# Kernel tuning notes

Measured on AMD Instinct MI355X. Metric: run time of the kernel, lower is better.

The kernel has to match this reference:

```python
import jax, jax.numpy as jnp
import numpy as np

HIDDEN = 768
HEADS = 12
HEAD_DIM = 64
SEQ = 512
DS_K = 64  # downsampling_k
EPS = 1e-6


def setup_inputs() -> dict:
    key = jax.random.key(0)
    ks = jax.random.split(key, 16)
    B = 32
    sd = 1.0 / DS_K
    glorot = jax.nn.initializers.lecun_normal()  # flax default_kernel_init
    inp = {
        "query": jax.random.normal(ks[0], (B, SEQ, HIDDEN), jnp.float32),
        "key": jax.random.normal(ks[1], (B, SEQ, HIDDEN), jnp.float32),
        "value": jax.random.normal(ks[2], (B, SEQ, HIDDEN), jnp.float32),
        "step": 0,
        # learned Linformer-style downsampling projections [k, s]
        "W_kds": sd * jax.random.normal(ks[3], (DS_K, SEQ), jnp.float32),
        "W_vds": sd * jax.random.normal(ks[4], (DS_K, SEQ), jnp.float32),
        # DenseGeneral qkv kernels [d, n, h] and biases [n, h]
        "Wq": glorot(ks[5], (HIDDEN, HEADS, HEAD_DIM), jnp.float32),
        "bq": jnp.zeros((HEADS, HEAD_DIM), jnp.float32),
        "Wk": glorot(ks[6], (HIDDEN, HEADS, HEAD_DIM), jnp.float32),
        "bk": jnp.zeros((HEADS, HEAD_DIM), jnp.float32),
        "Wv": glorot(ks[7], (HIDDEN, HEADS, HEAD_DIM), jnp.float32),
        "bv": jnp.zeros((HEADS, HEAD_DIM), jnp.float32),
        # out projection contracts (n, h) -> hidden
        "Wout": glorot(ks[8], (HEADS * HEAD_DIM, HIDDEN), jnp.float32).reshape(HEADS, HEAD_DIM, HIDDEN),
        "bout": jnp.zeros((HIDDEN,), jnp.float32),
    }
    return inp


def reference(query, key, value, step, W_kds, W_vds, Wq, bq, Wk, bk, Wv, bv, Wout, bout):
    # Linformer-style downsample of keys/values along sequence: [b,s,d] -> [b,k,d]
    key_ds = jnp.einsum("ks,bsd->bkd", W_kds, key)
    val_ds = jnp.einsum("ks,bsd->bkd", W_vds, value)

    # per-head projections
    queries = jnp.einsum("bqd,dnh->bqnh", query, Wq) + bq    # [b,q,n,h]
    keys = jnp.einsum("bkd,dnh->bknh", key_ds, Wk) + bk      # [b,k,n,h]
    values = jnp.einsum("bkd,dnh->bknh", val_ds, Wv) + bv    # [b,k,n,h]

    # kernelized linear attention with elu feature map (mask=False path)
    phi_q = jax.nn.elu(queries) + 1.0
    phi_k = jax.nn.elu(keys) + 1.0
    s = jnp.einsum("bknd,bknh->bndh", phi_k, values)          # [b,n,h,h] KV state
    z = jnp.sum(phi_k, axis=1)                                 # [b,n,h]
    qs = jnp.einsum("bqnd,bndh->bqnh", phi_q, s)
    qz = jnp.einsum("bqnd,bnd->bqn", phi_q, z) + EPS
    a_v = qs / qz[..., None]                                   # [b,q,n,h]

    out = jnp.einsum("bqnh,nhD->bqD", a_v, Wout) + bout        # [b,q,hidden]
    return out
```

## Files before the change

kernel.cpp:

```cpp
#include <hip/hip_runtime.h>

typedef unsigned short u16;
typedef u16 u16x8 __attribute__((ext_vector_type(8)));
typedef __bf16 bf16;
typedef bf16 bf16x8 __attribute__((ext_vector_type(8)));
typedef float f32x4 __attribute__((ext_vector_type(4)));

__device__ __forceinline__ float bf2f(u16 v) {
  union { unsigned u; float f; } x; x.u = ((unsigned)v) << 16; return x.f;
}
__device__ __forceinline__ u16 f2bf(float f) {
  union { float f; unsigned u; } x; x.f = f;
  unsigned u = x.u;
  u += 0x7fffu + ((u >> 16) & 1u);
  return (u16)(u >> 16);
}

#define GLDS16(g, l) __builtin_amdgcn_global_load_lds( \
    (const __attribute__((address_space(1))) unsigned int*)(const void*)(g), \
    (__attribute__((address_space(3))) unsigned int*)(void*)(l), 16, 0, 0)

__global__ __launch_bounds__(256, 4) void prepds_k(
    const float* __restrict__ Wq, const float* __restrict__ Wk,
    const float* __restrict__ Wv, const float* __restrict__ Wout,
    const float* __restrict__ query,
    const float* __restrict__ W_kds, const float* __restrict__ W_vds,
    const float* __restrict__ b0, const float* __restrict__ b1,
    const float* __restrict__ b2, const float* __restrict__ b3,
    const float* __restrict__ key, const float* __restrict__ value,
    u16* __restrict__ WT, u16* __restrict__ q_bf,
    u16* __restrict__ dstB, u16* __restrict__ key_ds)
{
  __shared__ u16 S[64 * 256];
  const int blk = blockIdx.x;
  const int t = threadIdx.x;

  if (blk < 768) {
    const int nt = (blk % 12) * 64;
    const int yb = blk / 12;
    const int pair = yb >> 5, b = yb & 31;
    const float* src = (pair ? value : key) + (size_t)b * 512 * 768;
    const float* W32 = pair ? W_vds : W_kds;
    u16* dst = key_ds + (size_t)pair * 1572864 + (size_t)b * 49152;
    const int wave = t >> 6, lane = t & 63;
    const int bn = lane;
    const int kl = wave * 64;
    const int sw = (bn & 7) << 3;
    const float* bcol = src + nt + bn;
    const int wm = (wave >> 1) * 32, wn = (wave & 1) * 32;
    const int lrow = lane & 15, quad = lane >> 4;
    f32x4 acc[2][2] = {};

    auto st16 = [&](const float* buf, int off) {
      #pragma unroll
      for (int g = 0; g < 2; ++g) {
        u16x8 wv;
        #pragma unroll
        for (int i = 0; i < 8; ++i) wv[i] = f2bf(buf[g * 8 + i]);
        *(u16x8*)&S[bn * 256 + ((kl + off + g * 8) ^ sw)] = wv;
      }
    };

    #pragma unroll
    for (int ph = 0; ph < 2; ++ph) {
      const int kb = ph * 256;
      if (ph) __syncthreads();
      float ba[16], bb[16];
      #pragma unroll
      for (int i = 0; i < 16; ++i) ba[i] = bcol[(size_t)(kb + kl + i) * 768];
      #pragma unroll
      for (int i = 0; i < 16; ++i) bb[i] = bcol[(size_t)(kb + kl + 16 + i) * 768];
      st16(ba, 0);
      #pragma unroll
      for (int i = 0; i < 16; ++i) ba[i] = bcol[(size_t)(kb + kl + 32 + i) * 768];
      st16(bb, 16);
      #pragma unroll
      for (int i = 0; i < 16; ++i) bb[i] = bcol[(size_t)(kb + kl + 48 + i) * 768];
      st16(ba, 32);
      st16(bb, 48);
      __syncthreads();
      #pragma unroll
      for (int step = 0; step < 8; ++step) {
        bf16x8 av2[2], bv[2];
        #pragma unroll
        for (int i = 0; i < 2; ++i) {
          const float* wr = &W32[(size_t)(wm + i * 16 + lrow) * 512 + kb + step * 32 + quad * 8];
          f32x4 w0 = *(const f32x4*)wr;
          f32x4 w1 = *(const f32x4*)(wr + 4);
          u16x8 aw;
          #pragma unroll
          for (int jj = 0; jj < 4; ++jj) { aw[jj] = f2bf(w0[jj]); aw[4 + jj] = f2bf(w1[jj]); }
          av2[i] = *(bf16x8*)&aw;
        }
        #pragma unroll
        for (int j = 0; j < 2; ++j) {
          const int n = wn + j * 16 + lrow;
          bv[j] = *(const bf16x8*)&S[n * 256 + ((step * 32 + quad * 8) ^ ((n & 7) << 3))];
        }
        #pragma unroll
        for (int i = 0; i < 2; ++i)
          #pragma unroll
          for (int j = 0; j < 2; ++j)
            acc[i][j] = __builtin_amdgcn_mfma_f32_16x16x32_bf16(av2[i], bv[j], acc[i][j], 0, 0, 0);
      }
    }
    #pragma unroll
    for (int i = 0; i < 2; ++i)
      #pragma unroll
      for (int j = 0; j < 2; ++j) {
        const int col = nt + wn + j * 16 + lrow;
        #pragma unroll
        for (int r = 0; r < 4; ++r) {
          const int row = wm + i * 16 + quad * 4 + r;
          dst[(size_t)row * 768 + col] = f2bf(acc[i][j][r]);
        }
      }
  } else if (blk < 1344) {
    u16 (*T)[72] = (u16(*)[72])S;
    const int tb = blk - 768;
    const int bz = tb / 144, rr = tb % 144;
    const int r0 = (rr / 12) * 64, c0 = (rr % 12) * 64;
    const float* W = (bz == 0) ? Wq : (bz == 1) ? Wk : (bz == 2) ? Wv : Wout;
    u16* O = WT + (size_t)bz * 768 * 768;
    #pragma unroll
    for (int p = 0; p < 2; ++p) {
      int v = t + p * 256;
      int r = v / 8, c = (v % 8) * 8;
      f32x4 x0 = *(const f32x4*)&W[(size_t)(r0 + r) * 768 + c0 + c];
      f32x4 x1 = *(const f32x4*)&W[(size_t)(r0 + r) * 768 + c0 + c + 4];
      #pragma unroll
      for (int i = 0; i < 4; ++i) { T[r][c + i] = f2bf(x0[i]); T[r][c + 4 + i] = f2bf(x1[i]); }
    }
    __syncthreads();
    #pragma unroll
    for (int p = 0; p < 2; ++p) {
      int v = t + p * 256;
      int r = v / 8, c = (v % 8) * 8;
      u16x8 tv;
      #pragma unroll
      for (int i = 0; i < 8; ++i) tv[i] = T[c + i][r];
      *(u16x8*)&O[(size_t)(c0 + r) * 768 + r0 + c] = tv;
    }
  } else if (blk < 7488) {
    const size_t i = (size_t)(blk - 1344) * 256 + t;
    f32x4 a = *(const f32x4*)&query[i * 8];
    f32x4 b = *(const f32x4*)&query[i * 8 + 4];
    u16x8 w;
    #pragma unroll
    for (int j = 0; j < 4; ++j) { w[j] = f2bf(a[j]); w[4 + j] = f2bf(b[j]); }
    *(u16x8*)&q_bf[i * 8] = w;
  } else {
    const int i = (blk - 7488) * 256 + t;
    if (i < 3072) {
      int s = i / 768, si = i % 768;
      const float* src = (s == 0) ? b0 : (s == 1) ? b1 : (s == 2) ? b2 : b3;
      dstB[i] = f2bf(src[si]);
    }
  }
}

template<int ACT, bool OF32>
__global__ __launch_bounds__(256) void gemm97_k(
    const u16* __restrict__ A, int lda,
    const u16* __restrict__ Bt, int ldb,
    void* __restrict__ Craw, int ldc,
    const u16* __restrict__ bias, int K)
{
  __shared__ u16 As[128 * 32];
  __shared__ u16 Bs[128 * 32];
  const int mt = blockIdx.x * 128, nt = blockIdx.y * 128;
  const int t = threadIdx.x, wave = t >> 6, lane = t & 63;
  const int wm = (wave >> 1) * 64, wn = (wave & 1) * 64;
  const int lrow = lane & 15, quad = lane >> 4;
  f32x4 acc[4][4] = {};

  for (int k0 = 0; k0 < K; k0 += 32) {
    __syncthreads();
    #pragma unroll
    for (int p = 0; p < 2; ++p) {
      const int s = wave * 128 + p * 64 + lane;
      const int r = s >> 2, c = (s & 3) * 8;
      const int lb = (wave * 128 + p * 64) * 8;
      GLDS16(&A[(size_t)(mt + r) * lda + k0 + c], &As[lb]);
      GLDS16(&Bt[(size_t)(nt + r) * ldb + k0 + c], &Bs[lb]);
    }
    __syncthreads();

    bf16x8 av[4], bv[4];
    #pragma unroll
    for (int i = 0; i < 4; ++i) av[i] = *(const bf16x8*)&As[(wm + i * 16 + lrow) * 32 + quad * 8];
    #pragma unroll
    for (int j = 0; j < 4; ++j) bv[j] = *(const bf16x8*)&Bs[(wn + j * 16 + lrow) * 32 + quad * 8];
    #pragma unroll
    for (int i = 0; i < 4; ++i)
      #pragma unroll
      for (int j = 0; j < 4; ++j)
        acc[i][j] = __builtin_amdgcn_mfma_f32_16x16x32_bf16(av[i], bv[j], acc[i][j], 0, 0, 0);
  }

  #pragma unroll
  for (int i = 0; i < 4; ++i) {
    #pragma unroll
    for (int j = 0; j < 4; ++j) {
      const int col = nt + wn + j * 16 + lrow;
      const float badd = bias ? bf2f(bias[col]) : 0.0f;
      #pragma unroll
      for (int r = 0; r < 4; ++r) {
        const int row = mt + wm + i * 16 + quad * 4 + r;
        float v = acc[i][j][r] + badd;
        if constexpr (ACT == 1) v = v > 0.0f ? v + 1.0f : __expf(v);
        if constexpr (OF32) ((float*)Craw)[(size_t)row * ldc + col] = v;
        else                ((u16*)Craw)[(size_t)row * ldc + col] = f2bf(v);
      }
    }
  }
}

template<int BM, int BN, int BK, int WM, int WN>
__global__ __launch_bounds__(256) void gemmkv_k(
    const u16* __restrict__ A, int lda,
    const u16* __restrict__ B, int ldb,
    u16* __restrict__ C, int ldc,
    const u16* __restrict__ bias,
    int K,
    long long offA_b, long long offB_b, long long offC_b, long long offBias_b)
{
  constexpr int LDSK = BK + 8;
  __shared__ u16 As[BM][LDSK];
  __shared__ u16 Bs[BN][LDSK];
  const int bb = blockIdx.z;
  A += bb * offA_b; B += bb * offB_b; C += bb * offC_b; bias += bb * offBias_b;
  const int mt = blockIdx.x * BM;
  const int nt = blockIdx.y * BN;
  const int t = threadIdx.x;
  const int wave = t >> 6, lane = t & 63;
  constexpr int WAVES_N = BN / WN;
  const int wm = (wave / WAVES_N) * WM;
  const int wn = (wave % WAVES_N) * WN;
  constexpr int FM = WM / 16, FN = WN / 16;
  const int lrow = lane & 15, quad = lane >> 4;
  f32x4 acc[FM][FN] = {};

  for (int k0 = 0; k0 < K; k0 += BK) {
    __syncthreads();
    #pragma unroll
    for (int p = 0; p < (BM * BK / 8) / 256; ++p) {
      int v = t + p * 256;
      int r = v / (BK / 8), c = (v % (BK / 8)) * 8;
      *(u16x8*)&As[r][c] = *(const u16x8*)&A[(size_t)(mt + r) * lda + k0 + c];
    }
    #pragma unroll
    for (int p = 0; p < (BN * BK / 8) / 256; ++p) {
      int v = t + p * 256;
      int r = v / (BK / 8), c = (v % (BK / 8)) * 8;
      *(u16x8*)&Bs[r][c] = *(const u16x8*)&B[(size_t)(nt + r) * ldb + k0 + c];
    }
    __syncthreads();
    bf16x8 av[FM], bv[FN];
    #pragma unroll
    for (int i = 0; i < FM; ++i) av[i] = *(const bf16x8*)&As[wm + i * 16 + lrow][quad * 8];
    #pragma unroll
    for (int j = 0; j < FN; ++j) bv[j] = *(const bf16x8*)&Bs[wn + j * 16 + lrow][quad * 8];
    #pragma unroll
    for (int i = 0; i < FM; ++i)
      #pragma unroll
      for (int j = 0; j < FN; ++j)
        acc[i][j] = __builtin_amdgcn_mfma_f32_16x16x32_bf16(av[i], bv[j], acc[i][j], 0, 0, 0);
  }
  #pragma unroll
  for (int i = 0; i < FM; ++i)
    #pragma unroll
    for (int j = 0; j < FN; ++j) {
      const int col = nt + wn + j * 16 + lrow;
      const float badd = bf2f(bias[col]);
      #pragma unroll
      for (int r = 0; r < 4; ++r) {
        const int row = mt + wm + i * 16 + quad * 4 + r;
        float v = acc[i][j][r] + badd;
        if (bb == 0) v = v > 0.0f ? v + 1.0f : __expf(v);
        C[(size_t)row * ldc + col] = f2bf(v);
      }
    }
}

__global__ __launch_bounds__(256) void kv_state_k(
    const u16* __restrict__ phi_k, const u16* __restrict__ vals,
    u16* __restrict__ sT, float* __restrict__ z)
{
  __shared__ float pk[64][65];
  __shared__ float vv[64][65];
  const int x = blockIdx.x;
  const int b = x / 12, n = x % 12;
  const int t = threadIdx.x;
  const u16* pkg = phi_k + (size_t)b * 64 * 768 + n * 64;
  const u16* vvg = vals  + (size_t)b * 64 * 768 + n * 64;
  #pragma unroll
  for (int p = 0; p < 2; ++p) {
    int v = t + p * 256;
    int r = v / 8, c = (v % 8) * 8;
    u16x8 a  = *(const u16x8*)&pkg[(size_t)r * 768 + c];
    u16x8 bq = *(const u16x8*)&vvg[(size_t)r * 768 + c];
    #pragma unroll
    for (int i = 0; i < 8; ++i) { pk[r][c + i] = bf2f(a[i]); vv[r][c + i] = bf2f(bq[i]); }
  }
  __syncthreads();
  const int d0 = (t >> 4) * 4, h0 = (t & 15) * 4;
  float s4[4][4] = {};
  for (int k = 0; k < 64; ++k) {
    float pv[4], vb[4];
    #pragma unroll
    for (int i = 0; i < 4; ++i) { pv[i] = pk[k][d0 + i]; vb[i] = vv[k][h0 + i]; }
    #pragma unroll
    for (int i = 0; i < 4; ++i)
      #pragma unroll
      for (int j = 0; j < 4; ++j) s4[i][j] += pv[i] * vb[j];
  }
  const size_t base = (size_t)x * 4096;
  #pragma unroll
  for (int i = 0; i < 4; ++i)
    #pragma unroll
    for (int j = 0; j < 4; ++j)
      sT[base + (size_t)(h0 + j) * 64 + d0 + i] = f2bf(s4[i][j]);
  if (t < 64) {
    float zz = 0.f;
    for (int k = 0; k < 64; ++k) zz += pk[k][t];
    z[(size_t)x * 64 + t] = zz;
  }
}

__global__ __launch_bounds__(256) void attn_av_k(
    u16* __restrict__ phi_q, const u16* __restrict__ sT, const float* __restrict__ zbuf)
{
  __shared__ u16 As[64 * 72];
  __shared__ u16 Bs[64 * 72];
  __shared__ float zv[64];
  __shared__ float zpart[4][64];
  __shared__ float zq[64];
  const int x = blockIdx.x, y = blockIdx.y;
  const int b = y / 12, n = y % 12;
  const int t = threadIdx.x;
  u16* Abase = phi_q + (size_t)b * 512 * 768 + (size_t)x * 64 * 768 + n * 64;
  const u16* Bbase = sT + (size_t)y * 4096;
  if (t < 64) zv[t] = zbuf[(size_t)y * 64 + t];
  #pragma unroll
  for (int p = 0; p < 2; ++p) {
    int v = t + p * 256;
    int r = v >> 3, c = (v & 7) * 8;
    *(u16x8*)&As[r * 72 + c] = *(const u16x8*)&Abase[(size_t)r * 768 + c];
    *(u16x8*)&Bs[r * 72 + c] = *(const u16x8*)&Bbase[r * 64 + c];
  }
  __syncthreads();
  {
    int r = t & 63, seg = t >> 6;
    float s = 0.f;
    #pragma unroll
    for (int j = 0; j < 16; ++j) s += bf2f(As[r * 72 + seg * 16 + j]) * zv[seg * 16 + j];
    zpart[seg][r] = s;
  }
  __syncthreads();
  if (t < 64) {
    float s = zpart[0][t] + zpart[1][t] + zpart[2][t] + zpart[3][t];
    zq[t] = 1.0f / (s + 1e-6f);
  }
  const int wave = t >> 6, lane = t & 63;
  const int wm = (wave >> 1) * 32, wn = (wave & 1) * 32;
  const int lrow = lane & 15, quad = lane >> 4;
  f32x4 acc[2][2] = {};
  #pragma unroll
  for (int c = 0; c < 2; ++c) {
    bf16x8 av[2], bv[2];
    #pragma unroll
    for (int i = 0; i < 2; ++i) av[i] = *(const bf16x8*)&As[(wm + i * 16 + lrow) * 72 + c * 32 + quad * 8];
    #pragma unroll
    for (int j = 0; j < 2; ++j) bv[j] = *(const bf16x8*)&Bs[(wn + j * 16 + lrow) * 72 + c * 32 + quad * 8];
    #pragma unroll
    for (int i = 0; i < 2; ++i)
      #pragma unroll
      for (int j = 0; j < 2; ++j)
        acc[i][j] = __builtin_amdgcn_mfma_f32_16x16x32_bf16(av[i], bv[j], acc[i][j], 0, 0, 0);
  }
  __syncthreads();
  #pragma unroll
  for (int i = 0; i < 2; ++i)
    #pragma unroll
    for (int j = 0; j < 2; ++j) {
      const int col = wn + j * 16 + lrow;
      #pragma unroll
      for (int r = 0; r < 4; ++r) {
        const int row = wm + i * 16 + quad * 4 + r;
        Abase[(size_t)row * 768 + col] = f2bf(acc[i][j][r] * zq[row]);
      }
    }
}

__global__ void tagfill_k(float* out, float val, int n) {
  int i = blockIdx.x * 256 + threadIdx.x;
  if (i < n) out[i] = val;
}

extern "C" void kernel_launch(void* const* d_in, const int* in_sizes, int n_in,
                              void* d_out, int out_size, void* d_ws, size_t ws_size,
                              hipStream_t stream) {
  (void)out_size;
  float* out = (float*)d_out;

  int o;
  if (n_in >= 14 && in_sizes[3] == 1) o = 4;
  else if (n_in == 13) o = 3;
  else { tagfill_k<<<4, 256, 0, stream>>>(out, 77.0f, 1024); return; }
  if (in_sizes[0] != 12582912 || in_sizes[o + 0] != 32768 || in_sizes[o + 2] != 589824) {
    tagfill_k<<<4, 256, 0, stream>>>(out, 88.0f, 1024); return;
  }

  const float* query = (const float*)d_in[0];
  const float* key   = (const float*)d_in[1];
  const float* value = (const float*)d_in[2];
  const float* W_kds = (const float*)d_in[o + 0];
  const float* W_vds = (const float*)d_in[o + 1];
  const float* Wq   = (const float*)d_in[o + 2];
  const float* bq   = (const float*)d_in[o + 3];
  const float* Wk   = (const float*)d_in[o + 4];
  const float* bk   = (const float*)d_in[o + 5];
  const float* Wv   = (const float*)d_in[o + 6];
  const float* bv   = (const float*)d_in[o + 7];
  const float* Wout = (const float*)d_in[o + 8];
  const float* bout = (const float*)d_in[o + 9];

  const size_t NEED = 61478912;
  if (ws_size < NEED) { tagfill_k<<<4, 256, 0, stream>>>(out, 123.0f, 1024); return; }

  char* base = (char*)d_ws;
  u16*   WT     = (u16*)base;
  char*  Breg   = base + 4718592;
  u16*   q_bf   = (u16*)Breg;
  u16*   sT     = (u16*)Breg;
  float* zbuf   = (float*)(Breg + 3145728);
  u16*   phi_k  = (u16*)(Breg + 6291456);
  u16*   vals   = (u16*)(Breg + 9437184);
  u16*   phi_q  = (u16*)(base + 29884416);
  u16*   bias_c = (u16*)(base + 55181312);
  u16*   key_ds = (u16*)(base + 55187456);
  u16* a_v = phi_q;
  u16* WqT   = WT;
  u16* WkT   = WT + 768 * 768;
  u16* WoutT = WT + 3 * 768 * 768;
  u16* bq_c = bias_c, *bk_c = bias_c + 768, *bout_c = bias_c + 2304;

  prepds_k<<<7500, 256, 0, stream>>>(Wq, Wk, Wv, Wout, query, W_kds, W_vds,
                                     bq, bk, bv, bout, key, value,
                                     WT, q_bf, bias_c, key_ds);

  gemm97_k<1, false><<<dim3(128, 6), 256, 0, stream>>>(
      q_bf, 768, WqT, 768, phi_q, 768, bq_c, 768);

  gemmkv_k<64, 64, 32, 32, 32><<<dim3(32, 12, 2), 256, 0, stream>>>(
      key_ds, 768, WkT, 768, phi_k, 768, bk_c, 768,
      1572864, 589824, 1572864, 768);

  kv_state_k<<<dim3(384), 256, 0, stream>>>(phi_k, vals, sT, zbuf);

  attn_av_k<<<dim3(8, 384), 256, 0, stream>>>(phi_q, sT, zbuf);

  gemm97_k<0, true><<<dim3(128, 6), 256, 0, stream>>>(
      a_v, 768, WoutT, 768, out, 768, bout_c, 768);
}
```

Measured before the change: 316.9 us.

## Fuse K/V projection with KV-state kernel and rework downsample staging

Merges the per-head K/V projection GEMM and the KV-state/z reduction into one kernel per (batch, head), so phi_k and values stay in LDS and never round-trip through global memory. This also drops one launch and uses MFMA for the state outer product. The downsample path in the prep kernel now stages fp32 key/value tiles with async global-to-LDS loads and pre-converts the W_ds rows to bf16 in LDS. Downsample blocks are interleaved with the conversion blocks (every tenth block) to spread the heavy work across the grid. In exchange, the fused kernel runs only 384 blocks, and bf16 conversion now happens per LDS read during the MFMA loop.

```diff
diff --git a/kernel.cpp b/kernel.cpp
--- a/kernel.cpp
+++ b/kernel.cpp
@@ -1,6 +1,7 @@
 #include <hip/hip_runtime.h>
 
 typedef unsigned short u16;
+typedef u16 u16x4 __attribute__((ext_vector_type(4)));
 typedef u16 u16x8 __attribute__((ext_vector_type(8)));
 typedef __bf16 bf16;
 typedef bf16 bf16x8 __attribute__((ext_vector_type(8)));
@@ -20,7 +21,7 @@
     (const __attribute__((address_space(1))) unsigned int*)(const void*)(g), \
     (__attribute__((address_space(3))) unsigned int*)(void*)(l), 16, 0, 0)
 
-__global__ __launch_bounds__(256, 4) void prepds_k(
+__global__ __launch_bounds__(256) void prepds_k(
     const float* __restrict__ Wq, const float* __restrict__ Wk,
     const float* __restrict__ Wv, const float* __restrict__ Wout,
     const float* __restrict__ query,
@@ -31,78 +32,70 @@
     u16* __restrict__ WT, u16* __restrict__ q_bf,
     u16* __restrict__ dstB, u16* __restrict__ key_ds)
 {
-  __shared__ u16 S[64 * 256];
+  __shared__ char sm[50176];
   const int blk = blockIdx.x;
   const int t = threadIdx.x;
 
-  if (blk < 768) {
-    const int nt = (blk % 12) * 64;
-    const int yb = blk / 12;
+  if (blk % 10 == 0) {
+    const int id = blk / 10;
+    float* Sg = (float*)sm;
+    u16* Wbf = (u16*)(sm + 32768);
+    const int nt = (id % 12) * 64;
+    const int yb = id / 12;
     const int pair = yb >> 5, b = yb & 31;
     const float* src = (pair ? value : key) + (size_t)b * 512 * 768;
     const float* W32 = pair ? W_vds : W_kds;
     u16* dst = key_ds + (size_t)pair * 1572864 + (size_t)b * 49152;
     const int wave = t >> 6, lane = t & 63;
-    const int bn = lane;
-    const int kl = wave * 64;
-    const int sw = (bn & 7) << 3;
-    const float* bcol = src + nt + bn;
     const int wm = (wave >> 1) * 32, wn = (wave & 1) * 32;
     const int lrow = lane & 15, quad = lane >> 4;
+    const int gr = lane >> 4;
+    const int gc = (lane & 15) * 16;
+    const int wrow = t >> 5;
+    const int wcol = (t & 31) * 4;
     f32x4 acc[2][2] = {};
 
-    auto st16 = [&](const float* buf, int off) {
-      #pragma unroll
-      for (int g = 0; g < 2; ++g) {
-        u16x8 wv;
-        #pragma unroll
-        for (int i = 0; i < 8; ++i) wv[i] = f2bf(buf[g * 8 + i]);
-        *(u16x8*)&S[bn * 256 + ((kl + off + g * 8) ^ sw)] = wv;
-      }
-    };
-
-    #pragma unroll
-    for (int ph = 0; ph < 2; ++ph) {
-      const int kb = ph * 256;
-      if (ph) __syncthreads();
-      float ba[16], bb[16];
-      #pragma unroll
-      for (int i = 0; i < 16; ++i) ba[i] = bcol[(size_t)(kb + kl + i) * 768];
-      #pragma unroll
-      for (int i = 0; i < 16; ++i) bb[i] = bcol[(size_t)(kb + kl + 16 + i) * 768];
-      st16(ba, 0);
-      #pragma unroll
-      for (int i = 0; i < 16; ++i) ba[i] = bcol[(size_t)(kb + kl + 32 + i) * 768];
-      st16(bb, 16);
-      #pragma unroll
-      for (int i = 0; i < 16; ++i) bb[i] = bcol[(size_t)(kb + kl + 48 + i) * 768];
-      st16(ba, 32);
-      st16(bb, 48);
+    for (int ph = 0; ph < 4; ++ph) {
+      const int kb = ph * 128;
+      #pragma unroll
+      for (int j = 0; j < 8; ++j) {
+        const int idx = wave * 8 + j;
+        const float* gsrc = src + (size_t)(kb + idx * 4 + gr) * 768 + nt;
+        GLDS16((const char*)gsrc + gc, (char*)Sg + idx * 1024);
+      }
+      f32x4 wr[8];
+      #pragma unroll
+      for (int i = 0; i < 8; ++i)
+        wr[i] = *(const f32x4*)&W32[(size_t)(i * 8 + wrow) * 512 + kb + wcol];
+      #pragma unroll
+      for (int i = 0; i < 8; ++i) {
+        u16x4 wv4;
+        #pragma unroll
+        for (int q2 = 0; q2 < 4; ++q2) wv4[q2] = f2bf(wr[i][q2]);
+        *(u16x4*)&Wbf[(i * 8 + wrow) * 136 + wcol] = wv4;
+      }
       __syncthreads();
       #pragma unroll
-      for (int step = 0; step < 8; ++step) {
-        bf16x8 av2[2], bv[2];
-        #pragma unroll
-        for (int i = 0; i < 2; ++i) {
-          const float* wr = &W32[(size_t)(wm + i * 16 + lrow) * 512 + kb + step * 32 + quad * 8];
-          f32x4 w0 = *(const f32x4*)wr;
-          f32x4 w1 = *(const f32x4*)(wr + 4);
-          u16x8 aw;
+      for (int s = 0; s < 4; ++s) {
+        bf16x8 av[2], bv[2];
+        #pragma unroll
+        for (int i = 0; i < 2; ++i)
+          av[i] = *(const bf16x8*)&Wbf[(wm + i * 16 + lrow) * 136 + s * 32 + quad * 8];
+        #pragma unroll
+        for (int j = 0; j < 2; ++j) {
+          const int n2 = wn + j * 16 + lrow;
+          u16x8 bb;
           #pragma unroll
-          for (int jj = 0; jj < 4; ++jj) { aw[jj] = f2bf(w0[jj]); aw[4 + jj] = f2bf(w1[jj]); }
-          av2[i] = *(bf16x8*)&aw;
-        }
-        #pragma unroll
-        for (int j = 0; j < 2; ++j) {
-          const int n = wn + j * 16 + lrow;
-          bv[j] = *(const bf16x8*)&S[n * 256 + ((step * 32 + quad * 8) ^ ((n & 7) << 3))];
+          for (int e = 0; e < 8; ++e) bb[e] = f2bf(Sg[(s * 32 + quad * 8 + e) * 64 + n2]);
+          bv[j] = *(bf16x8*)&bb;
         }
         #pragma unroll
         for (int i = 0; i < 2; ++i)
           #pragma unroll
           for (int j = 0; j < 2; ++j)
-            acc[i][j] = __builtin_amdgcn_mfma_f32_16x16x32_bf16(av2[i], bv[j], acc[i][j], 0, 0, 0);
-      }
+            acc[i][j] = __builtin_amdgcn_mfma_f32_16x16x32_bf16(av[i], bv[j], acc[i][j], 0, 0, 0);
+      }
+      __syncthreads();
     }
     #pragma unroll
     for (int i = 0; i < 2; ++i)
@@ -115,10 +108,13 @@
           dst[(size_t)row * 768 + col] = f2bf(acc[i][j][r]);
         }
       }
-  } else if (blk < 1344) {
-    u16 (*T)[72] = (u16(*)[72])S;
-    const int tb = blk - 768;
-    const int bz = tb / 144, rr = tb % 144;
+    return;
+  }
+
+  const int pid = blk - blk / 10 - 1;
+  if (pid < 576) {
+    u16 (*T)[72] = (u16(*)[72])sm;
+    const int bz = pid / 144, rr = pid % 144;
     const int r0 = (rr / 12) * 64, c0 = (rr % 12) * 64;
     const float* W = (bz == 0) ? Wq : (bz == 1) ? Wk : (bz == 2) ? Wv : Wout;
     u16* O = WT + (size_t)bz * 768 * 768;
@@ -141,21 +137,140 @@
       for (int i = 0; i < 8; ++i) tv[i] = T[c + i][r];
       *(u16x8*)&O[(size_t)(c0 + r) * 768 + r0 + c] = tv;
     }
-  } else if (blk < 7488) {
-    const size_t i = (size_t)(blk - 1344) * 256 + t;
+  } else if (pid < 6720) {
+    const size_t i = (size_t)(pid - 576) * 256 + t;
     f32x4 a = *(const f32x4*)&query[i * 8];
     f32x4 b = *(const f32x4*)&query[i * 8 + 4];
     u16x8 w;
     #pragma unroll
     for (int j = 0; j < 4; ++j) { w[j] = f2bf(a[j]); w[4 + j] = f2bf(b[j]); }
     *(u16x8*)&q_bf[i * 8] = w;
-  } else {
-    const int i = (blk - 7488) * 256 + t;
+  } else if (pid < 6732) {
+    const int i = (pid - 6720) * 256 + t;
     if (i < 3072) {
       int s = i / 768, si = i % 768;
       const float* src = (s == 0) ? b0 : (s == 1) ? b1 : (s == 2) ? b2 : b3;
       dstB[i] = f2bf(src[si]);
     }
+  }
+}
+
+__global__ __launch_bounds__(256) void fkv_k(
+    const u16* __restrict__ key_ds,
+    const u16* __restrict__ WT,
+    const u16* __restrict__ bias_c,
+    u16* __restrict__ sT, float* __restrict__ z)
+{
+  __shared__ char sm[32768];
+  u16* T0 = (u16*)sm;
+  u16* Pt = (u16*)sm;
+  u16* Vt = (u16*)(sm + 9216);
+  const int x = blockIdx.x;
+  const int b = x / 12, n = x % 12;
+  const int t = threadIdx.x, wave = t >> 6, lane = t & 63;
+  const u16* srcs[4] = {
+    key_ds + (size_t)b * 49152,
+    WT + 589824 + (size_t)n * 49152,
+    key_ds + 1572864 + (size_t)b * 49152,
+    WT + 2 * 589824 + (size_t)n * 49152 };
+  const int grow = lane >> 3;
+  const int gchunk = (lane & 7) ^ (grow & 7);
+  const int isV = wave & 1;
+  const int wm = (wave >> 1) * 32;
+  const u16* Atile_s = srcs[isV ? 2 : 0];
+  (void)Atile_s;
+  const u16* Asrc = srcs[isV ? 2 : 0];
+  const u16* Bsrc = srcs[isV ? 3 : 1];
+  (void)Asrc; (void)Bsrc;
+  u16* Atile = T0 + (isV ? 2 : 0) * 4096;
+  u16* Btile = T0 + (isV ? 3 : 1) * 4096;
+  const int lrow = lane & 15, quad = lane >> 4;
+  f32x4 acc[2][4] = {};
+
+  for (int k0 = 0; k0 < 768; k0 += 64) {
+    const u16* s = srcs[wave];
+    u16* dtile = T0 + wave * 4096;
+    #pragma unroll
+    for (int j = 0; j < 8; ++j) {
+      const u16* gsrc = s + (size_t)(j * 8 + grow) * 768 + k0 + gchunk * 8;
+      GLDS16(gsrc, (char*)dtile + j * 1024);
+    }
+    __syncthreads();
+    #pragma unroll
+    for (int c = 0; c < 2; ++c) {
+      bf16x8 av[2], bv[4];
+      #pragma unroll
+      for (int i = 0; i < 2; ++i) {
+        const int row = wm + i * 16 + lrow;
+        av[i] = *(const bf16x8*)&Atile[row * 64 + (((c * 4 + quad) ^ (row & 7)) * 8)];
+      }
+      #pragma unroll
+      for (int j = 0; j < 4; ++j) {
+        const int row = j * 16 + lrow;
+        bv[j] = *(const bf16x8*)&Btile[row * 64 + (((c * 4 + quad) ^ (row & 7)) * 8)];
+      }
+      #pragma unroll
+      for (int i = 0; i < 2; ++i)
+        #pragma unroll
+        for (int j = 0; j < 4; ++j)
+          acc[i][j] = __builtin_amdgcn_mfma_f32_16x16x32_bf16(av[i], bv[j], acc[i][j], 0, 0, 0);
+    }
+    __syncthreads();
+  }
+
+  const u16* bias = bias_c + (isV ? 1536 : 768) + n * 64;
+  u16* Ttile = isV ? Vt : Pt;
+  #pragma unroll
+  for (int i = 0; i < 2; ++i)
+    #pragma unroll
+    for (int j = 0; j < 4; ++j) {
+      const int col = j * 16 + lrow;
+      const float badd = bf2f(bias[col]);
+      u16x4 pk4;
+      #pragma unroll
+      for (int r = 0; r < 4; ++r) {
+        float v = acc[i][j][r] + badd;
+        if (!isV) v = v > 0.0f ? v + 1.0f : __expf(v);
+        pk4[r] = f2bf(v);
+      }
+      *(u16x4*)&Ttile[col * 72 + wm + i * 16 + quad * 4] = pk4;
+    }
+  __syncthreads();
+
+  const int wm2 = (wave >> 1) * 32, wn2 = (wave & 1) * 32;
+  f32x4 a2[2][2] = {};
+  #pragma unroll
+  for (int c = 0; c < 2; ++c) {
+    bf16x8 av[2], bv[2];
+    #pragma unroll
+    for (int i = 0; i < 2; ++i)
+      av[i] = *(const bf16x8*)&Vt[(wm2 + i * 16 + lrow) * 72 + c * 32 + quad * 8];
+    #pragma unroll
+    for (int j = 0; j < 2; ++j)
+      bv[j] = *(const bf16x8*)&Pt[(wn2 + j * 16 + lrow) * 72 + c * 32 + quad * 8];
+    #pragma unroll
+    for (int i = 0; i < 2; ++i)
+      #pragma unroll
+      for (int j = 0; j < 2; ++j)
+        a2[i][j] = __builtin_amdgcn_mfma_f32_16x16x32_bf16(av[i], bv[j], a2[i][j], 0, 0, 0);
+  }
+  u16* sTg = sT + (size_t)x * 4096;
+  #pragma unroll
+  for (int i = 0; i < 2; ++i)
+    #pragma unroll
+    for (int j = 0; j < 2; ++j)
+      #pragma unroll
+      for (int r = 0; r < 4; ++r)
+        sTg[(size_t)(wm2 + i * 16 + quad * 4 + r) * 64 + wn2 + j * 16 + lrow] = f2bf(a2[i][j][r]);
+  if (t < 64) {
+    float zz = 0.f;
+    #pragma unroll
+    for (int g = 0; g < 8; ++g) {
+      u16x8 p = *(const u16x8*)&Pt[t * 72 + g * 8];
+      #pragma unroll
+      for (int e = 0; e < 8; ++e) zz += bf2f(p[e]);
+    }
+    z[(size_t)x * 64 + t] = zz;
   }
 }
 
@@ -216,118 +331,6 @@
   }
 }
 
-template<int BM, int BN, int BK, int WM, int WN>
-__global__ __launch_bounds__(256) void gemmkv_k(
-    const u16* __restrict__ A, int lda,
-    const u16* __restrict__ B, int ldb,
-    u16* __restrict__ C, int ldc,
-    const u16* __restrict__ bias,
-    int K,
-    long long offA_b, long long offB_b, long long offC_b, long long offBias_b)
-{
-  constexpr int LDSK = BK + 8;
-  __shared__ u16 As[BM][LDSK];
-  __shared__ u16 Bs[BN][LDSK];
-  const int bb = blockIdx.z;
-  A += bb * offA_b; B += bb * offB_b; C += bb * offC_b; bias += bb * offBias_b;
-  const int mt = blockIdx.x * BM;
-  const int nt = blockIdx.y * BN;
-  const int t = threadIdx.x;
-  const int wave = t >> 6, lane = t & 63;
-  constexpr int WAVES_N = BN / WN;
-  const int wm = (wave / WAVES_N) * WM;
-  const int wn = (wave % WAVES_N) * WN;
-  constexpr int FM = WM / 16, FN = WN / 16;
-  const int lrow = lane & 15, quad = lane >> 4;
-  f32x4 acc[FM][FN] = {};
-
-  for (int k0 = 0; k0 < K; k0 += BK) {
-    __syncthreads();
-    #pragma unroll
-    for (int p = 0; p < (BM * BK / 8) / 256; ++p) {
-      int v = t + p * 256;
-      int r = v / (BK / 8), c = (v % (BK / 8)) * 8;
-      *(u16x8*)&As[r][c] = *(const u16x8*)&A[(size_t)(mt + r) * lda + k0 + c];
-    }
-    #pragma unroll
-    for (int p = 0; p < (BN * BK / 8) / 256; ++p) {
-      int v = t + p * 256;
-      int r = v / (BK / 8), c = (v % (BK / 8)) * 8;
-      *(u16x8*)&Bs[r][c] = *(const u16x8*)&B[(size_t)(nt + r) * ldb + k0 + c];
-    }
-    __syncthreads();
-    bf16x8 av[FM], bv[FN];
-    #pragma unroll
-    for (int i = 0; i < FM; ++i) av[i] = *(const bf16x8*)&As[wm + i * 16 + lrow][quad * 8];
-    #pragma unroll
-    for (int j = 0; j < FN; ++j) bv[j] = *(const bf16x8*)&Bs[wn + j * 16 + lrow][quad * 8];
-    #pragma unroll
-    for (int i = 0; i < FM; ++i)
-      #pragma unroll
-      for (int j = 0; j < FN; ++j)
-        acc[i][j] = __builtin_amdgcn_mfma_f32_16x16x32_bf16(av[i], bv[j], acc[i][j], 0, 0, 0);
-  }
-  #pragma unroll
-  for (int i = 0; i < FM; ++i)
-    #pragma unroll
-    for (int j = 0; j < FN; ++j) {
-      const int col = nt + wn + j * 16 + lrow;
-      const float badd = bf2f(bias[col]);
-      #pragma unroll
-      for (int r = 0; r < 4; ++r) {
-        const int row = mt + wm + i * 16 + quad * 4 + r;
-        float v = acc[i][j][r] + badd;
-        if (bb == 0) v = v > 0.0f ? v + 1.0f : __expf(v);
-        C[(size_t)row * ldc + col] = f2bf(v);
-      }
-    }
-}
-
-__global__ __launch_bounds__(256) void kv_state_k(
-    const u16* __restrict__ phi_k, const u16* __restrict__ vals,
-    u16* __restrict__ sT, float* __restrict__ z)
-{
-  __shared__ float pk[64][65];
-  __shared__ float vv[64][65];
-  const int x = blockIdx.x;
-  const int b = x / 12, n = x % 12;
-  const int t = threadIdx.x;
-  const u16* pkg = phi_k + (size_t)b * 64 * 768 + n * 64;
-  const u16* vvg = vals  + (size_t)b * 64 * 768 + n * 64;
-  #pragma unroll
-  for (int p = 0; p < 2; ++p) {
-    int v = t + p * 256;
-    int r = v / 8, c = (v % 8) * 8;
-    u16x8 a  = *(const u16x8*)&pkg[(size_t)r * 768 + c];
-    u16x8 bq = *(const u16x8*)&vvg[(size_t)r * 768 + c];
-    #pragma unroll
-    for (int i = 0; i < 8; ++i) { pk[r][c + i] = bf2f(a[i]); vv[r][c + i] = bf2f(bq[i]); }
-  }
-  __syncthreads();
-  const int d0 = (t >> 4) * 4, h0 = (t & 15) * 4;
-  float s4[4][4] = {};
-  for (int k = 0; k < 64; ++k) {
-    float pv[4], vb[4];
-    #pragma unroll
-    for (int i = 0; i < 4; ++i) { pv[i] = pk[k][d0 + i]; vb[i] = vv[k][h0 + i]; }
-    #pragma unroll
-    for (int i = 0; i < 4; ++i)
-      #pragma unroll
-      for (int j = 0; j < 4; ++j) s4[i][j] += pv[i] * vb[j];
-  }
-  const size_t base = (size_t)x * 4096;
-  #pragma unroll
-  for (int i = 0; i < 4; ++i)
-    #pragma unroll
-    for (int j = 0; j < 4; ++j)
-      sT[base + (size_t)(h0 + j) * 64 + d0 + i] = f2bf(s4[i][j]);
-  if (t < 64) {
-    float zz = 0.f;
-    for (int k = 0; k < 64; ++k) zz += pk[k][t];
-    z[(size_t)x * 64 + t] = zz;
-  }
-}
-
 __global__ __launch_bounds__(256) void attn_av_k(
     u16* __restrict__ phi_q, const u16* __restrict__ sT, const float* __restrict__ zbuf)
 {
@@ -435,29 +438,22 @@
   u16*   q_bf   = (u16*)Breg;
   u16*   sT     = (u16*)Breg;
   float* zbuf   = (float*)(Breg + 3145728);
-  u16*   phi_k  = (u16*)(Breg + 6291456);
-  u16*   vals   = (u16*)(Breg + 9437184);
   u16*   phi_q  = (u16*)(base + 29884416);
   u16*   bias_c = (u16*)(base + 55181312);
   u16*   key_ds = (u16*)(base + 55187456);
   u16* a_v = phi_q;
   u16* WqT   = WT;
-  u16* WkT   = WT + 768 * 768;
   u16* WoutT = WT + 3 * 768 * 768;
-  u16* bq_c = bias_c, *bk_c = bias_c + 768, *bout_c = bias_c + 2304;
-
-  prepds_k<<<7500, 256, 0, stream>>>(Wq, Wk, Wv, Wout, query, W_kds, W_vds,
+  u16* bq_c = bias_c, *bout_c = bias_c + 2304;
+
+  prepds_k<<<7680, 256, 0, stream>>>(Wq, Wk, Wv, Wout, query, W_kds, W_vds,
                                      bq, bk, bv, bout, key, value,
                                      WT, q_bf, bias_c, key_ds);
 
   gemm97_k<1, false><<<dim3(128, 6), 256, 0, stream>>>(
       q_bf, 768, WqT, 768, phi_q, 768, bq_c, 768);
 
-  gemmkv_k<64, 64, 32, 32, 32><<<dim3(32, 12, 2), 256, 0, stream>>>(
-      key_ds, 768, WkT, 768, phi_k, 768, bk_c, 768,
-      1572864, 589824, 1572864, 768);
-
-  kv_state_k<<<dim3(384), 256, 0, stream>>>(phi_k, vals, sT, zbuf);
+  fkv_k<<<384, 256, 0, stream>>>(key_ds, WT, bias_c, sT, zbuf);
 
   attn_av_k<<<dim3(8, 384), 256, 0, stream>>>(phi_q, sT, zbuf);
 
```

New measurement: 318.2 us. About the same (+0.4%).
